# Kernel tuning notes

Measured on AMD Instinct MI355X. Metric: run time of the kernel, lower is better.

## Reference

```python
import jax, jax.numpy as jnp
import numpy as np

B, N, C_IN = 4, 2048, 64
HID, HEADS, NQ = 128, 4, 16
D = HID // HEADS  # per-head dim = 32
NEG_SLOPE = 0.2
MASK_VAL = -1e9


def setup_inputs() -> dict:
    key = jax.random.key(0)
    ks = jax.random.split(key, 8)
    x = jax.random.normal(ks[0], (B, N, C_IN), dtype=jnp.float32)
    adj = jax.random.randint(ks[1], (N, N), 0, 2, dtype=jnp.int32)
    # lin_in: Linear(in_channels, hidden_dim)
    W_in = jax.random.normal(ks[2], (C_IN, HID), dtype=jnp.float32) / np.sqrt(C_IN)
    b_in = jnp.zeros((HID,), dtype=jnp.float32)
    # attention vectors [1, heads, d]
    att_src = jax.random.normal(ks[3], (1, HEADS, D), dtype=jnp.float32) * 0.1
    att_dst = jax.random.normal(ks[4], (1, HEADS, D), dtype=jnp.float32) * 0.1
    # output_head: Linear(num_nodes*hidden_dim, num_qubits)
    W_out = jax.random.normal(ks[5], (N * HID, NQ), dtype=jnp.float32) / np.sqrt(N * HID)
    b_out = jnp.zeros((NQ,), dtype=jnp.float32)
    return {"x": x, "adj": adj, "W_in": W_in, "b_in": b_in,
            "att_src": att_src, "att_dst": att_dst,
            "W_out": W_out, "b_out": b_out}


def reference(x, adj, W_in, b_in, att_src, att_dst, W_out, b_out):
    b, n, _ = x.shape
    h = (x @ W_in + b_in).reshape(b, n, HEADS, D)          # [B,N,H,D]
    alpha_src = jnp.sum(h * att_src, axis=-1)               # [B,N,H]
    alpha_dst = jnp.sum(h * att_dst, axis=-1)               # [B,N,H]
    # additive scores: score[b,i,j,h] = src[b,i,h] + dst[b,j,h]
    scores = alpha_src[:, :, None, :] + alpha_dst[:, None, :, :]  # [B,N,N,H]
    scores = jnp.where(scores >= 0, scores, NEG_SLOPE * scores)   # leaky relu
    mask = (adj == 0)[None, :, :, None]                     # [1,N,N,1]
    scores = jnp.where(mask, MASK_VAL, scores)
    alpha = jax.nn.softmax(scores, axis=2)                  # softmax over neighbors j
    # dropout p=0.0 (eval) -> identity
    out = jnp.einsum('bijh,bjhd->bihd', alpha, h)           # [B,N,H,D]
    out = out.reshape(b, n * HEADS * D)                     # [B, N*HID]
    return out @ W_out + b_out                              # [B, NQ]
```

## Files before the change

### kernel.cpp

```cpp
#include <hip/hip_runtime.h>
#include <math.h>

#define BB 4
#define NN 2048
#define CIN 64
#define HID 128
#define HEADS 4
#define NQ 16
#define KTOT (NN*HID)
#define LOG2E 1.44269504088896340736f
#define NSL 4
#define HB 512
#define AB 2048

typedef __attribute__((ext_vector_type(8))) _Float16 half8;
typedef __attribute__((ext_vector_type(4))) float f32x4;
typedef __attribute__((ext_vector_type(4))) unsigned uint4v;

__global__ __launch_bounds__(256) void k_pre(
    const float* __restrict__ x, const float* __restrict__ W_in,
    const float* __restrict__ b_in, const float* __restrict__ att_src,
    const float* __restrict__ att_dst, const int* __restrict__ adj,
    _Float16* __restrict__ hHT, float* __restrict__ EsA, float* __restrict__ Es5A,
    float* __restrict__ EdA, float* __restrict__ Ed5A,
    unsigned* __restrict__ adjT, const float* __restrict__ b_out,
    float* __restrict__ dout)
{
    __shared__ float Wl[CIN * HID];
    __shared__ float xl[16][CIN];
    const int t = threadIdx.x;

    if (blockIdx.x >= HB) {
        const int bid = blockIdx.x - HB;
        if (bid == 0 && t < 64) dout[t] = b_out[t & 15];
        const int gid = bid * 256 + t;
        const int lane = t & 63;
        const int4* p = (const int4*)(adj + (size_t)gid * 8);
        const int4 a = p[0], b = p[1];
        unsigned byte =
            (a.x != 0 ? 1u : 0u)  | (a.y != 0 ? 2u : 0u)  | (a.z != 0 ? 4u : 0u)  | (a.w != 0 ? 8u : 0u) |
            (b.x != 0 ? 16u : 0u) | (b.y != 0 ? 32u : 0u) | (b.z != 0 ? 64u : 0u) | (b.w != 0 ? 128u : 0u);
        unsigned u = byte | (((unsigned)__shfl_xor((int)byte, 1, 64)) << 8);
        u = u | (((unsigned)__shfl_xor((int)u, 2, 64)) << 16);
        if ((lane & 3) == 0) {
            const int widx = gid >> 2;
            const int i = widx >> 6, jw = widx & 63;
            adjT[(size_t)jw * NN + i] = u;
        }
        return;
    }

    const int jj0 = blockIdx.x * 16;
    {
        const float4* Ws = (const float4*)W_in;
        float4* Wd = (float4*)Wl;
#pragma unroll
        for (int u = 0; u < 8; ++u) Wd[t + 256 * u] = Ws[t + 256 * u];
        ((float4*)&xl[0][0])[t] = ((const float4*)(x + (size_t)jj0 * CIN))[t];
    }
    __syncthreads();

    const int c = t & 127, rg = t >> 7;
    const int b = jj0 >> 11, j0 = (jj0 & (NN - 1)) + rg * 8;
    const int h = c >> 5;

    float acc[8];
    const float bc = b_in[c];
#pragma unroll
    for (int rr = 0; rr < 8; ++rr) acc[rr] = bc;

#pragma unroll
    for (int k4 = 0; k4 < CIN; k4 += 4) {
        const float w0 = Wl[(k4 + 0) * HID + c];
        const float w1 = Wl[(k4 + 1) * HID + c];
        const float w2 = Wl[(k4 + 2) * HID + c];
        const float w3 = Wl[(k4 + 3) * HID + c];
#pragma unroll
        for (int rr = 0; rr < 8; ++rr) {
            const float4 xv = *(const float4*)&xl[rg * 8 + rr][k4];
            acc[rr] = fmaf(xv.w, w3, fmaf(xv.z, w2, fmaf(xv.y, w1, fmaf(xv.x, w0, acc[rr]))));
        }
    }

    half8 hv;
#pragma unroll
    for (int rr = 0; rr < 8; ++rr) hv[rr] = (_Float16)acc[rr];
    *(half8*)(hHT + (size_t)b * KTOT + (size_t)(j0 >> 5) * 4096 + c * 32 + (j0 & 31)) = hv;

    const float as = att_src[c], ad = att_dst[c];
#pragma unroll
    for (int rr = 0; rr < 8; ++rr) {
        float vs = acc[rr] * as, vd = acc[rr] * ad;
#pragma unroll
        for (int m = 16; m >= 1; m >>= 1) {
            vs += __shfl_xor(vs, m, 64);
            vd += __shfl_xor(vd, m, 64);
        }
        if ((t & 31) == 0) {
            const size_t idx = (size_t)(b * HEADS + h) * NN + j0 + rr;
            const float s2 = vs * LOG2E, d2 = vd * LOG2E;
            EsA[idx]  = __builtin_amdgcn_exp2f(s2);
            Es5A[idx] = __builtin_amdgcn_exp2f(0.2f * s2);
            EdA[idx]  = __builtin_amdgcn_exp2f(d2);
            Ed5A[idx] = __builtin_amdgcn_exp2f(0.2f * d2);
        }
    }
}

__global__ __launch_bounds__(256, 4) void k_attn(
    const unsigned* __restrict__ adjT, const _Float16* __restrict__ hHT,
    const float* __restrict__ EsA, const float* __restrict__ Es5A,
    const float* __restrict__ EdA, const float* __restrict__ Ed5A,
    _Float16* __restrict__ P, float* __restrict__ S)
{
    const int t = threadIdx.x;
    const int lane = t & 63;
    const int h = t >> 6;
    const int bx = blockIdx.x;
    const int iq = bx & 63;
    const int b = (bx >> 6) & 3;
    const int jq = bx >> 8;
    const int i0 = iq * 32;
    const int jb0 = jq * 16;

    const int r16 = lane & 15;
    const int g = lane >> 4;

    const size_t abase = (size_t)(b * HEADS + h) * NN;
    const float es0  = EsA [abase + i0 + r16];
    const float es05 = Es5A[abase + i0 + r16];
    const float es1  = EsA [abase + i0 + 16 + r16];
    const float es15 = Es5A[abase + i0 + 16 + r16];
    const unsigned* adjr0 = adjT + (size_t)jb0 * NN + i0 + r16;
    const unsigned* adjr1 = adjr0 + 16;
    const _Float16* hb = hHT + (size_t)b * KTOT + (size_t)jb0 * 4096
                             + (h * 32 + r16) * 32 + g * 8;
    const float4* ed4  = (const float4*)(EdA  + abase + jq * 512) + 2 * g;
    const float4* ed54 = (const float4*)(Ed5A + abase + jq * 512) + 2 * g;

    f32x4 acc00 = {0.f, 0.f, 0.f, 0.f};
    f32x4 acc01 = {0.f, 0.f, 0.f, 0.f};
    f32x4 acc10 = {0.f, 0.f, 0.f, 0.f};
    f32x4 acc11 = {0.f, 0.f, 0.f, 0.f};
    f32x4 accS0 = {0.f, 0.f, 0.f, 0.f};
    f32x4 accS1 = {0.f, 0.f, 0.f, 0.f};
    const half8 ones = {(_Float16)1.f, (_Float16)1.f, (_Float16)1.f, (_Float16)1.f,
                        (_Float16)1.f, (_Float16)1.f, (_Float16)1.f, (_Float16)1.f};

    auto MAKEAF = [&](float es, float es5, unsigned bits,
                      const float* edv, const float* ed5v) -> half8 {
        float wv[8];
#pragma unroll
        for (int e = 0; e < 8; ++e) {
            const float wp = es * edv[e];
            const float wn = es5 * ed5v[e];
            const float w = fmaxf(wp, wn);
            const unsigned m = (unsigned)(((int)(bits << (31 - e))) >> 31);
            wv[e] = __builtin_bit_cast(float, __builtin_bit_cast(unsigned, w) & m);
        }
        uint4v uu;
        uu[0] = __builtin_bit_cast(unsigned, __builtin_amdgcn_cvt_pkrtz(wv[0], wv[1]));
        uu[1] = __builtin_bit_cast(unsigned, __builtin_amdgcn_cvt_pkrtz(wv[2], wv[3]));
        uu[2] = __builtin_bit_cast(unsigned, __builtin_amdgcn_cvt_pkrtz(wv[4], wv[5]));
        uu[3] = __builtin_bit_cast(unsigned, __builtin_amdgcn_cvt_pkrtz(wv[6], wv[7]));
        return __builtin_bit_cast(half8, uu);
    };

    auto COMPUTE = [&](unsigned w0, unsigned w1, half8 bb0, half8 bb1,
                       float4 e0, float4 e1, float4 f0, float4 f1) {
        const float edv[8]  = {e0.x, e0.y, e0.z, e0.w, e1.x, e1.y, e1.z, e1.w};
        const float ed5v[8] = {f0.x, f0.y, f0.z, f0.w, f1.x, f1.y, f1.z, f1.w};
        const half8 af0 = MAKEAF(es0, es05, w0 >> (8 * g), edv, ed5v);
        const half8 af1 = MAKEAF(es1, es15, w1 >> (8 * g), edv, ed5v);
        acc00 = __builtin_amdgcn_mfma_f32_16x16x32_f16(af0, bb0, acc00, 0, 0, 0);
        acc01 = __builtin_amdgcn_mfma_f32_16x16x32_f16(af0, bb1, acc01, 0, 0, 0);
        accS0 = __builtin_amdgcn_mfma_f32_16x16x32_f16(af0, ones, accS0, 0, 0, 0);
        acc10 = __builtin_amdgcn_mfma_f32_16x16x32_f16(af1, bb0, acc10, 0, 0, 0);
        acc11 = __builtin_amdgcn_mfma_f32_16x16x32_f16(af1, bb1, acc11, 0, 0, 0);
        accS1 = __builtin_amdgcn_mfma_f32_16x16x32_f16(af1, ones, accS1, 0, 0, 0);
    };

    unsigned wA0 = adjr0[0], wA1 = adjr1[0];
    half8 bA0 = *(const half8*)(hb);
    half8 bA1 = *(const half8*)(hb + 512);
    float4 eA0 = ed4[0], eA1 = ed4[1];
    float4 fA0 = ed54[0], fA1 = ed54[1];
    __builtin_amdgcn_sched_barrier(0);

#pragma unroll 1
    for (int p = 0; p < 8; ++p) {
        const int nB = 2 * p + 1;
        const unsigned wB0 = adjr0[(size_t)nB * NN];
        const unsigned wB1 = adjr1[(size_t)nB * NN];
        const half8 bB0 = *(const half8*)(hb + nB * 4096);
        const half8 bB1 = *(const half8*)(hb + nB * 4096 + 512);
        const float4 eB0 = ed4[nB * 8],  eB1 = ed4[nB * 8 + 1];
        const float4 fB0 = ed54[nB * 8], fB1 = ed54[nB * 8 + 1];
        __builtin_amdgcn_sched_barrier(0);

        COMPUTE(wA0, wA1, bA0, bA1, eA0, eA1, fA0, fA1);
        __builtin_amdgcn_sched_barrier(0);

        if (p < 7) {
            const int nA = 2 * p + 2;
            wA0 = adjr0[(size_t)nA * NN];
            wA1 = adjr1[(size_t)nA * NN];
            bA0 = *(const half8*)(hb + nA * 4096);
            bA1 = *(const half8*)(hb + nA * 4096 + 512);
            eA0 = ed4[nA * 8];  eA1 = ed4[nA * 8 + 1];
            fA0 = ed54[nA * 8]; fA1 = ed54[nA * 8 + 1];
        }
        __builtin_amdgcn_sched_barrier(0);

        COMPUTE(wB0, wB1, bB0, bB1, eB0, eB1, fB0, fB1);
        __builtin_amdgcn_sched_barrier(0);
    }

    const size_t prow0 = (size_t)(jq * BB + b) * NN + i0;
#pragma unroll
    for (int r = 0; r < 4; ++r) {
        const size_t row0 = prow0 + 4 * g + r;
        const size_t row1 = prow0 + 16 + 4 * g + r;
        P[row0 * HID + h * 32 + r16]      = (_Float16)acc00[r];
        P[row0 * HID + h * 32 + 16 + r16] = (_Float16)acc01[r];
        P[row1 * HID + h * 32 + r16]      = (_Float16)acc10[r];
        P[row1 * HID + h * 32 + 16 + r16] = (_Float16)acc11[r];
        if (r16 == 0) {
            S[row0 * HEADS + h] = accS0[r];
            S[row1 * HEADS + h] = accS1[r];
        }
    }
}

__global__ __launch_bounds__(256) void k_proj(
    const _Float16* __restrict__ P, const float* __restrict__ S,
    const float* __restrict__ W_out, float* __restrict__ dout)
{
    __shared__ float wlT[NQ][260];
    __shared__ float red[256];

    const int t = threadIdx.x;
    const int k0 = blockIdx.x * 256;

#pragma unroll
    for (int u = 0; u < 4; ++u) {
        const int flat = (u * 256 + t) * 4;
        const float4 wv = *(const float4*)(W_out + (size_t)k0 * NQ + flat);
        const int krel = flat >> 4;
        const int q0 = flat & 15;
        wlT[q0 + 0][krel] = wv.x;
        wlT[q0 + 1][krel] = wv.y;
        wlT[q0 + 2][krel] = wv.z;
        wlT[q0 + 3][krel] = wv.w;
    }
    __syncthreads();

    const int q = t & 15;
    const int b = (t >> 4) & 3;
    const int ks = (t >> 6) * 64;
    const int i = (k0 + ks) >> 7;

    const _Float16* p0 = P + (size_t)(0 * BB + b) * KTOT + k0 + ks;
    const _Float16* p1 = P + (size_t)(1 * BB + b) * KTOT + k0 + ks;
    const _Float16* p2 = P + (size_t)(2 * BB + b) * KTOT + k0 + ks;
    const _Float16* p3 = P + (size_t)(3 * BB + b) * KTOT + k0 + ks;

    float acc = 0.f;
#pragma unroll
    for (int seg = 0; seg < 2; ++seg) {
        const int h = ((k0 + ks + seg * 32) >> 5) & 3;
        float rs = 0.f;
#pragma unroll
        for (int s = 0; s < NSL; ++s)
            rs += S[((size_t)(s * BB + b) * NN + i) * HEADS + h];
        const float inv = __builtin_amdgcn_rcpf(rs);
#pragma unroll
        for (int k8 = 0; k8 < 4; ++k8) {
            const int kk = seg * 32 + k8 * 8;
            const half8 a0 = *(const half8*)(p0 + kk);
            const half8 a1 = *(const half8*)(p1 + kk);
            const half8 a2 = *(const half8*)(p2 + kk);
            const half8 a3 = *(const half8*)(p3 + kk);
            const float4 w0 = *(const float4*)&wlT[q][ks + kk];
            const float4 w1 = *(const float4*)&wlT[q][ks + kk + 4];
            const float wf[8] = {w0.x, w0.y, w0.z, w0.w, w1.x, w1.y, w1.z, w1.w};
#pragma unroll
            for (int e = 0; e < 8; ++e) {
                const float ev = ((float)a0[e] + (float)a1[e]) + ((float)a2[e] + (float)a3[e]);
                acc = fmaf(ev * inv, wf[e], acc);
            }
        }
    }

    red[t] = acc;
    __syncthreads();
    if (t < 64)
        atomicAdd(&dout[t], red[t] + red[t + 64] + red[t + 128] + red[t + 192]);
}

extern "C" void kernel_launch(void* const* d_in, const int* in_sizes, int n_in,
                              void* d_out, int out_size, void* d_ws, size_t ws_size,
                              hipStream_t stream)
{
    const float* x       = (const float*)d_in[0];
    const int*   adj     = (const int*)d_in[1];
    const float* W_in    = (const float*)d_in[2];
    const float* b_in    = (const float*)d_in[3];
    const float* att_src = (const float*)d_in[4];
    const float* att_dst = (const float*)d_in[5];
    const float* W_out   = (const float*)d_in[6];
    const float* b_out   = (const float*)d_in[7];
    float* out = (float*)d_out;

    char* ws = (char*)d_ws;
    _Float16* P = (_Float16*)ws;
    float* S    = (float*)(ws + sizeof(_Float16) * (size_t)NSL * BB * KTOT);
    float* EsA  = S + (size_t)NSL * BB * NN * HEADS;
    float* Es5A = EsA  + (size_t)BB * HEADS * NN;
    float* EdA  = Es5A + (size_t)BB * HEADS * NN;
    float* Ed5A = EdA  + (size_t)BB * HEADS * NN;
    _Float16* hHT = (_Float16*)(Ed5A + (size_t)BB * HEADS * NN);
    unsigned* adjT = (unsigned*)((char*)hHT + sizeof(_Float16) * (size_t)BB * KTOT);

    k_pre<<<HB + AB, 256, 0, stream>>>(x, W_in, b_in, att_src, att_dst, adj,
                                       hHT, EsA, Es5A, EdA, Ed5A, adjT, b_out, out);
    k_attn<<<NSL * BB * (NN / 32), 256, 0, stream>>>(adjT, hHT, EsA, Es5A, EdA, Ed5A, P, S);
    k_proj<<<KTOT / 256, 256, 0, stream>>>(P, S, W_out, out);
}
```

Baseline: 71.24 us.

## Fuse three kernels into one cooperative persistent kernel with grid syncs

Merges the precompute, attention and projection kernels into a single cooperative launch of 512 blocks. Each block runs several virtual blocks per phase, and the phases are separated by grid.sync. This is meant to remove the launch gaps and tail effects between the three kernels. In exchange, each block does more sequential work, the 36KB shared buffer may limit occupancy, and a grid-wide barrier is added. The old three-kernel path remains as a fallback when cooperative launch is unavailable.

```diff
diff --git a/kernel.cpp b/kernel.cpp
--- a/kernel.cpp
+++ b/kernel.cpp
@@ -1,4 +1,5 @@
 #include <hip/hip_runtime.h>
+#include <hip/hip_cooperative_groups.h>
 #include <math.h>
 
 #define BB 4
@@ -10,6 +11,7 @@
 #define KTOT (NN*HID)
 #define LOG2E 1.44269504088896340736f
 #define NSL 4
+#define GRID 512
 #define HB 512
 #define AB 2048
 
@@ -17,109 +19,39 @@
 typedef __attribute__((ext_vector_type(4))) float f32x4;
 typedef __attribute__((ext_vector_type(4))) unsigned uint4v;
 
-__global__ __launch_bounds__(256) void k_pre(
-    const float* __restrict__ x, const float* __restrict__ W_in,
-    const float* __restrict__ b_in, const float* __restrict__ att_src,
-    const float* __restrict__ att_dst, const int* __restrict__ adj,
-    _Float16* __restrict__ hHT, float* __restrict__ EsA, float* __restrict__ Es5A,
-    float* __restrict__ EdA, float* __restrict__ Ed5A,
-    unsigned* __restrict__ adjT, const float* __restrict__ b_out,
-    float* __restrict__ dout)
-{
-    __shared__ float Wl[CIN * HID];
-    __shared__ float xl[16][CIN];
-    const int t = threadIdx.x;
-
-    if (blockIdx.x >= HB) {
-        const int bid = blockIdx.x - HB;
-        if (bid == 0 && t < 64) dout[t] = b_out[t & 15];
-        const int gid = bid * 256 + t;
-        const int lane = t & 63;
-        const int4* p = (const int4*)(adj + (size_t)gid * 8);
-        const int4 a = p[0], b = p[1];
-        unsigned byte =
-            (a.x != 0 ? 1u : 0u)  | (a.y != 0 ? 2u : 0u)  | (a.z != 0 ? 4u : 0u)  | (a.w != 0 ? 8u : 0u) |
-            (b.x != 0 ? 16u : 0u) | (b.y != 0 ? 32u : 0u) | (b.z != 0 ? 64u : 0u) | (b.w != 0 ? 128u : 0u);
-        unsigned u = byte | (((unsigned)__shfl_xor((int)byte, 1, 64)) << 8);
-        u = u | (((unsigned)__shfl_xor((int)u, 2, 64)) << 16);
-        if ((lane & 3) == 0) {
-            const int widx = gid >> 2;
-            const int i = widx >> 6, jw = widx & 63;
-            adjT[(size_t)jw * NN + i] = u;
-        }
-        return;
-    }
-
-    const int jj0 = blockIdx.x * 16;
-    {
-        const float4* Ws = (const float4*)W_in;
-        float4* Wd = (float4*)Wl;
-#pragma unroll
-        for (int u = 0; u < 8; ++u) Wd[t + 256 * u] = Ws[t + 256 * u];
-        ((float4*)&xl[0][0])[t] = ((const float4*)(x + (size_t)jj0 * CIN))[t];
-    }
-    __syncthreads();
-
-    const int c = t & 127, rg = t >> 7;
-    const int b = jj0 >> 11, j0 = (jj0 & (NN - 1)) + rg * 8;
-    const int h = c >> 5;
-
-    float acc[8];
-    const float bc = b_in[c];
-#pragma unroll
-    for (int rr = 0; rr < 8; ++rr) acc[rr] = bc;
-
-#pragma unroll
-    for (int k4 = 0; k4 < CIN; k4 += 4) {
-        const float w0 = Wl[(k4 + 0) * HID + c];
-        const float w1 = Wl[(k4 + 1) * HID + c];
-        const float w2 = Wl[(k4 + 2) * HID + c];
-        const float w3 = Wl[(k4 + 3) * HID + c];
-#pragma unroll
-        for (int rr = 0; rr < 8; ++rr) {
-            const float4 xv = *(const float4*)&xl[rg * 8 + rr][k4];
-            acc[rr] = fmaf(xv.w, w3, fmaf(xv.z, w2, fmaf(xv.y, w1, fmaf(xv.x, w0, acc[rr]))));
-        }
-    }
-
-    half8 hv;
-#pragma unroll
-    for (int rr = 0; rr < 8; ++rr) hv[rr] = (_Float16)acc[rr];
-    *(half8*)(hHT + (size_t)b * KTOT + (size_t)(j0 >> 5) * 4096 + c * 32 + (j0 & 31)) = hv;
-
-    const float as = att_src[c], ad = att_dst[c];
-#pragma unroll
-    for (int rr = 0; rr < 8; ++rr) {
-        float vs = acc[rr] * as, vd = acc[rr] * ad;
-#pragma unroll
-        for (int m = 16; m >= 1; m >>= 1) {
-            vs += __shfl_xor(vs, m, 64);
-            vd += __shfl_xor(vd, m, 64);
-        }
-        if ((t & 31) == 0) {
-            const size_t idx = (size_t)(b * HEADS + h) * NN + j0 + rr;
-            const float s2 = vs * LOG2E, d2 = vd * LOG2E;
-            EsA[idx]  = __builtin_amdgcn_exp2f(s2);
-            Es5A[idx] = __builtin_amdgcn_exp2f(0.2f * s2);
-            EdA[idx]  = __builtin_amdgcn_exp2f(d2);
-            Ed5A[idx] = __builtin_amdgcn_exp2f(0.2f * d2);
-        }
-    }
-}
-
-__global__ __launch_bounds__(256, 4) void k_attn(
-    const unsigned* __restrict__ adjT, const _Float16* __restrict__ hHT,
+namespace cg = cooperative_groups;
+
+__device__ __forceinline__ half8 makeaf_fac(float es, float es5, unsigned bits,
+                                            const float* edv, const float* ed5v)
+{
+    float wv[8];
+#pragma unroll
+    for (int e = 0; e < 8; ++e) {
+        const float wp = es * edv[e];
+        const float wn = es5 * ed5v[e];
+        const float w = fmaxf(wp, wn);
+        const unsigned m = (unsigned)(((int)(bits << (31 - e))) >> 31);
+        wv[e] = __builtin_bit_cast(float, __builtin_bit_cast(unsigned, w) & m);
+    }
+    uint4v uu;
+    uu[0] = __builtin_bit_cast(unsigned, __builtin_amdgcn_cvt_pkrtz(wv[0], wv[1]));
+    uu[1] = __builtin_bit_cast(unsigned, __builtin_amdgcn_cvt_pkrtz(wv[2], wv[3]));
+    uu[2] = __builtin_bit_cast(unsigned, __builtin_amdgcn_cvt_pkrtz(wv[4], wv[5]));
+    uu[3] = __builtin_bit_cast(unsigned, __builtin_amdgcn_cvt_pkrtz(wv[6], wv[7]));
+    return __builtin_bit_cast(half8, uu);
+}
+
+__device__ __forceinline__ void attn_body(
+    int vb, int t, const unsigned* __restrict__ adjT, const _Float16* __restrict__ hHT,
     const float* __restrict__ EsA, const float* __restrict__ Es5A,
     const float* __restrict__ EdA, const float* __restrict__ Ed5A,
     _Float16* __restrict__ P, float* __restrict__ S)
 {
-    const int t = threadIdx.x;
     const int lane = t & 63;
     const int h = t >> 6;
-    const int bx = blockIdx.x;
-    const int iq = bx & 63;
-    const int b = (bx >> 6) & 3;
-    const int jq = bx >> 8;
+    const int iq = vb & 63;
+    const int b = (vb >> 6) & 3;
+    const int jq = vb >> 8;
     const int i0 = iq * 32;
     const int jb0 = jq * 16;
 
@@ -147,31 +79,12 @@
     const half8 ones = {(_Float16)1.f, (_Float16)1.f, (_Float16)1.f, (_Float16)1.f,
                         (_Float16)1.f, (_Float16)1.f, (_Float16)1.f, (_Float16)1.f};
 
-    auto MAKEAF = [&](float es, float es5, unsigned bits,
-                      const float* edv, const float* ed5v) -> half8 {
-        float wv[8];
-#pragma unroll
-        for (int e = 0; e < 8; ++e) {
-            const float wp = es * edv[e];
-            const float wn = es5 * ed5v[e];
-            const float w = fmaxf(wp, wn);
-            const unsigned m = (unsigned)(((int)(bits << (31 - e))) >> 31);
-            wv[e] = __builtin_bit_cast(float, __builtin_bit_cast(unsigned, w) & m);
-        }
-        uint4v uu;
-        uu[0] = __builtin_bit_cast(unsigned, __builtin_amdgcn_cvt_pkrtz(wv[0], wv[1]));
-        uu[1] = __builtin_bit_cast(unsigned, __builtin_amdgcn_cvt_pkrtz(wv[2], wv[3]));
-        uu[2] = __builtin_bit_cast(unsigned, __builtin_amdgcn_cvt_pkrtz(wv[4], wv[5]));
-        uu[3] = __builtin_bit_cast(unsigned, __builtin_amdgcn_cvt_pkrtz(wv[6], wv[7]));
-        return __builtin_bit_cast(half8, uu);
-    };
-
     auto COMPUTE = [&](unsigned w0, unsigned w1, half8 bb0, half8 bb1,
                        float4 e0, float4 e1, float4 f0, float4 f1) {
         const float edv[8]  = {e0.x, e0.y, e0.z, e0.w, e1.x, e1.y, e1.z, e1.w};
         const float ed5v[8] = {f0.x, f0.y, f0.z, f0.w, f1.x, f1.y, f1.z, f1.w};
-        const half8 af0 = MAKEAF(es0, es05, w0 >> (8 * g), edv, ed5v);
-        const half8 af1 = MAKEAF(es1, es15, w1 >> (8 * g), edv, ed5v);
+        const half8 af0 = makeaf_fac(es0, es05, w0 >> (8 * g), edv, ed5v);
+        const half8 af1 = makeaf_fac(es1, es15, w1 >> (8 * g), edv, ed5v);
         acc00 = __builtin_amdgcn_mfma_f32_16x16x32_f16(af0, bb0, acc00, 0, 0, 0);
         acc01 = __builtin_amdgcn_mfma_f32_16x16x32_f16(af0, bb1, acc01, 0, 0, 0);
         accS0 = __builtin_amdgcn_mfma_f32_16x16x32_f16(af0, ones, accS0, 0, 0, 0);
@@ -232,15 +145,98 @@
     }
 }
 
-__global__ __launch_bounds__(256) void k_proj(
-    const _Float16* __restrict__ P, const float* __restrict__ S,
-    const float* __restrict__ W_out, float* __restrict__ dout)
-{
-    __shared__ float wlT[NQ][260];
-    __shared__ float red[256];
-
-    const int t = threadIdx.x;
-    const int k0 = blockIdx.x * 256;
+__device__ __forceinline__ void hidden_body(
+    int hbid, int t, char* smem,
+    const float* __restrict__ x, const float* __restrict__ W_in,
+    const float* __restrict__ b_in, const float* __restrict__ att_src,
+    const float* __restrict__ att_dst, _Float16* __restrict__ hHT,
+    float* __restrict__ EsA, float* __restrict__ Es5A,
+    float* __restrict__ EdA, float* __restrict__ Ed5A)
+{
+    float* Wl = (float*)smem;
+    float (*xl)[CIN] = (float(*)[CIN])(smem + 32768);
+    const int jj0 = hbid * 16;
+    {
+        const float4* Ws = (const float4*)W_in;
+        float4* Wd = (float4*)Wl;
+#pragma unroll
+        for (int u = 0; u < 8; ++u) Wd[t + 256 * u] = Ws[t + 256 * u];
+        ((float4*)&xl[0][0])[t] = ((const float4*)(x + (size_t)jj0 * CIN))[t];
+    }
+    __syncthreads();
+
+    const int c = t & 127, rg = t >> 7;
+    const int b = jj0 >> 11, j0 = (jj0 & (NN - 1)) + rg * 8;
+    const int h = c >> 5;
+
+    float acc[8];
+    const float bc = b_in[c];
+#pragma unroll
+    for (int rr = 0; rr < 8; ++rr) acc[rr] = bc;
+
+#pragma unroll
+    for (int k4 = 0; k4 < CIN; k4 += 4) {
+        const float w0 = Wl[(k4 + 0) * HID + c];
+        const float w1 = Wl[(k4 + 1) * HID + c];
+        const float w2 = Wl[(k4 + 2) * HID + c];
+        const float w3 = Wl[(k4 + 3) * HID + c];
+#pragma unroll
+        for (int rr = 0; rr < 8; ++rr) {
+            const float4 xv = *(const float4*)&xl[rg * 8 + rr][k4];
+            acc[rr] = fmaf(xv.w, w3, fmaf(xv.z, w2, fmaf(xv.y, w1, fmaf(xv.x, w0, acc[rr]))));
+        }
+    }
+
+    half8 hv;
+#pragma unroll
+    for (int rr = 0; rr < 8; ++rr) hv[rr] = (_Float16)acc[rr];
+    *(half8*)(hHT + (size_t)b * KTOT + (size_t)(j0 >> 5) * 4096 + c * 32 + (j0 & 31)) = hv;
+
+    const float as = att_src[c], ad = att_dst[c];
+#pragma unroll
+    for (int rr = 0; rr < 8; ++rr) {
+        float vs = acc[rr] * as, vd = acc[rr] * ad;
+#pragma unroll
+        for (int m = 16; m >= 1; m >>= 1) {
+            vs += __shfl_xor(vs, m, 64);
+            vd += __shfl_xor(vd, m, 64);
+        }
+        if ((t & 31) == 0) {
+            const size_t idx = (size_t)(b * HEADS + h) * NN + j0 + rr;
+            const float s2 = vs * LOG2E, d2 = vd * LOG2E;
+            EsA[idx]  = __builtin_amdgcn_exp2f(s2);
+            Es5A[idx] = __builtin_amdgcn_exp2f(0.2f * s2);
+            EdA[idx]  = __builtin_amdgcn_exp2f(d2);
+            Ed5A[idx] = __builtin_amdgcn_exp2f(0.2f * d2);
+        }
+    }
+}
+
+__device__ __forceinline__ void adjitem_body(int gid, int lane, const int* __restrict__ adj,
+                                             unsigned* __restrict__ adjT)
+{
+    const int4* p = (const int4*)(adj + (size_t)gid * 8);
+    const int4 a = p[0], b = p[1];
+    unsigned byte =
+        (a.x != 0 ? 1u : 0u)  | (a.y != 0 ? 2u : 0u)  | (a.z != 0 ? 4u : 0u)  | (a.w != 0 ? 8u : 0u) |
+        (b.x != 0 ? 16u : 0u) | (b.y != 0 ? 32u : 0u) | (b.z != 0 ? 64u : 0u) | (b.w != 0 ? 128u : 0u);
+    unsigned v = byte | (((unsigned)__shfl_xor((int)byte, 1, 64)) << 8);
+    v = v | (((unsigned)__shfl_xor((int)v, 2, 64)) << 16);
+    if ((lane & 3) == 0) {
+        const int widx = gid >> 2;
+        const int i = widx >> 6, jw = widx & 63;
+        adjT[(size_t)jw * NN + i] = v;
+    }
+}
+
+__device__ __forceinline__ void proj_body(
+    int vb, int t, char* smem, const _Float16* __restrict__ P,
+    const float* __restrict__ S, const float* __restrict__ W_out,
+    float* __restrict__ dout)
+{
+    float (*wlT)[260] = (float(*)[260])smem;
+    float* red = (float*)(smem + 16640);
+    const int k0 = vb * 256;
 
 #pragma unroll
     for (int u = 0; u < 4; ++u) {
@@ -296,6 +292,76 @@
     __syncthreads();
     if (t < 64)
         atomicAdd(&dout[t], red[t] + red[t + 64] + red[t + 128] + red[t + 192]);
+    __syncthreads();
+}
+
+__global__ __launch_bounds__(256, 4) void k_fused(
+    const float* __restrict__ x, const float* __restrict__ W_in,
+    const float* __restrict__ b_in, const float* __restrict__ att_src,
+    const float* __restrict__ att_dst, const int* __restrict__ adj,
+    const float* __restrict__ W_out, const float* __restrict__ b_out,
+    _Float16* __restrict__ hHT, float* __restrict__ EsA, float* __restrict__ Es5A,
+    float* __restrict__ EdA, float* __restrict__ Ed5A, unsigned* __restrict__ adjT,
+    _Float16* __restrict__ P, float* __restrict__ S, float* __restrict__ dout)
+{
+    cg::grid_group grid = cg::this_grid();
+    __shared__ __align__(16) char smem[36864];
+    const int t = threadIdx.x;
+    const int bid = blockIdx.x;
+    const int lane = t & 63;
+
+    hidden_body(bid, t, smem, x, W_in, b_in, att_src, att_dst, hHT, EsA, Es5A, EdA, Ed5A);
+#pragma unroll
+    for (int u = 0; u < 4; ++u)
+        adjitem_body(bid * 1024 + u * 256 + t, lane, adj, adjT);
+    if (bid == 0 && t < 64) dout[t] = b_out[t & 15];
+
+    grid.sync();
+
+    attn_body(bid,       t, adjT, hHT, EsA, Es5A, EdA, Ed5A, P, S);
+    attn_body(bid + 512, t, adjT, hHT, EsA, Es5A, EdA, Ed5A, P, S);
+
+    grid.sync();
+
+    proj_body(bid,       t, smem, P, S, W_out, dout);
+    proj_body(bid + 512, t, smem, P, S, W_out, dout);
+}
+
+__global__ __launch_bounds__(256) void kf_pre(
+    const float* __restrict__ x, const float* __restrict__ W_in,
+    const float* __restrict__ b_in, const float* __restrict__ att_src,
+    const float* __restrict__ att_dst, const int* __restrict__ adj,
+    _Float16* __restrict__ hHT, float* __restrict__ EsA, float* __restrict__ Es5A,
+    float* __restrict__ EdA, float* __restrict__ Ed5A,
+    unsigned* __restrict__ adjT, const float* __restrict__ b_out,
+    float* __restrict__ dout)
+{
+    __shared__ __align__(16) char smem[36864];
+    const int t = threadIdx.x;
+    if (blockIdx.x >= HB) {
+        const int bid = blockIdx.x - HB;
+        if (bid == 0 && t < 64) dout[t] = b_out[t & 15];
+        adjitem_body(bid * 256 + t, t & 63, adj, adjT);
+        return;
+    }
+    hidden_body(blockIdx.x, t, smem, x, W_in, b_in, att_src, att_dst, hHT, EsA, Es5A, EdA, Ed5A);
+}
+
+__global__ __launch_bounds__(256, 4) void kf_attn(
+    const unsigned* __restrict__ adjT, const _Float16* __restrict__ hHT,
+    const float* __restrict__ EsA, const float* __restrict__ Es5A,
+    const float* __restrict__ EdA, const float* __restrict__ Ed5A,
+    _Float16* __restrict__ P, float* __restrict__ S)
+{
+    attn_body(blockIdx.x, threadIdx.x, adjT, hHT, EsA, Es5A, EdA, Ed5A, P, S);
+}
+
+__global__ __launch_bounds__(256) void kf_proj(
+    const _Float16* __restrict__ P, const float* __restrict__ S,
+    const float* __restrict__ W_out, float* __restrict__ dout)
+{
+    __shared__ __align__(16) char smem[17664];
+    proj_body(blockIdx.x, threadIdx.x, smem, P, S, W_out, dout);
 }
 
 extern "C" void kernel_launch(void* const* d_in, const int* in_sizes, int n_in,
@@ -322,8 +388,37 @@
     _Float16* hHT = (_Float16*)(Ed5A + (size_t)BB * HEADS * NN);
     unsigned* adjT = (unsigned*)((char*)hHT + sizeof(_Float16) * (size_t)BB * KTOT);
 
-    k_pre<<<HB + AB, 256, 0, stream>>>(x, W_in, b_in, att_src, att_dst, adj,
-                                       hHT, EsA, Es5A, EdA, Ed5A, adjT, b_out, out);
-    k_attn<<<NSL * BB * (NN / 32), 256, 0, stream>>>(adjT, hHT, EsA, Es5A, EdA, Ed5A, P, S);
-    k_proj<<<KTOT / 256, 256, 0, stream>>>(P, S, W_out, out);
-}
+    static int coop_ok = -1;
+    if (coop_ok < 0) {
+        int dev = 0; hipGetDevice(&dev);
+        int coop = 0, ncu = 0, mb = 0;
+        hipDeviceGetAttribute(&coop, hipDeviceAttributeCooperativeLaunch, dev);
+        hipDeviceGetAttribute(&ncu, hipDeviceAttributeMultiprocessorCount, dev);
+        hipOccupancyMaxActiveBlocksPerMultiprocessor(&mb, (const void*)k_fused, 256, 0);
+        coop_ok = (coop && (long)mb * ncu >= GRID) ? 1 : 0;
+    }
+
+    bool done = false;
+    if (coop_ok == 1) {
+        const float* xx = x; const float* wi = W_in; const float* bi = b_in;
+        const float* as_ = att_src; const float* ad_ = att_dst; const int* aj = adj;
+        const float* wo = W_out; const float* bo = b_out;
+        _Float16* hh = hHT; float* e1 = EsA; float* e2 = Es5A; float* e3 = EdA; float* e4 = Ed5A;
+        unsigned* at = adjT; _Float16* pp = P; float* ss = S; float* oo = out;
+        void* kargs[] = {
+            &xx, &wi, &bi, &as_, &ad_, &aj, &wo, &bo,
+            &hh, &e1, &e2, &e3, &e4, &at, &pp, &ss, &oo
+        };
+        hipError_t e = hipLaunchCooperativeKernel((void*)k_fused, dim3(GRID), dim3(256),
+                                                  kargs, 0, stream);
+        if (e == hipSuccess) done = true;
+        else coop_ok = 0;
+    }
+
+    if (!done) {
+        kf_pre<<<HB + AB, 256, 0, stream>>>(x, W_in, b_in, att_src, att_dst, adj,
+                                            hHT, EsA, Es5A, EdA, Ed5A, adjT, b_out, out);
+        kf_attn<<<NSL * BB * (NN / 32), 256, 0, stream>>>(adjT, hHT, EsA, Es5A, EdA, Ed5A, P, S);
+        kf_proj<<<KTOT / 256, 256, 0, stream>>>(P, S, W_out, out);
+    }
+}
```

Measured after the change: 197.6 us. 177% more time.
